# Optimization experiments

Hardware: AMD Instinct MI355X
Metric: run time of the kernel (lower is better)

## Reference

```python
import jax, jax.numpy as jnp
import numpy as np

# Module config (mirrors TritonMoEConfig)
N_EMBD = 768
EXPERT_SIZES = [(8, 512), (8, 1024)]  # (count, width) pairs
TOP_K = 8
NORM_TOPK_PROB = True

EXPERT_WIDTHS = []
for cnt, w in EXPERT_SIZES:
    EXPERT_WIDTHS += [w] * cnt
EXPERT_OFFSETS = np.concatenate([[0], np.cumsum(EXPERT_WIDTHS)]).astype(np.int64)
NUM_EXPERTS = len(EXPERT_WIDTHS)          # 16
TOTAL_WIDTH = int(EXPERT_OFFSETS[-1])     # 12288


def setup_inputs() -> dict:
    key = jax.random.key(0)
    k1, k2, k3, k4 = jax.random.split(key, 4)
    x = jax.random.normal(k1, (1, 2048, N_EMBD), dtype=jnp.float32)
    # trunc_normal(std=0.02) approximated by clipped normal
    router_w = jax.random.normal(k2, (NUM_EXPERTS, N_EMBD), dtype=jnp.float32) * 0.02
    w1 = jnp.clip(jax.random.normal(k3, (N_EMBD, TOTAL_WIDTH), dtype=jnp.float32) * 0.02, -0.06, 0.06)
    w2 = jnp.clip(jax.random.normal(k4, (TOTAL_WIDTH, N_EMBD), dtype=jnp.float32) * 0.02, -0.06, 0.06)
    return {"x": x, "router_w": router_w, "w1": w1, "w2": w2}


def reference(x, router_w, w1, w2):
    B, S, D = x.shape
    xt = x.reshape(-1, D)                              # [T, D]
    T = xt.shape[0]
    # 1. Route tokens: softmax over experts, top-k selection
    logits = jnp.einsum('td,ed->te', xt, router_w)     # [T, E]
    probs = jax.nn.softmax(logits, axis=-1)
    topk_w, topk_idx = jax.lax.top_k(probs, TOP_K)     # [T, K]
    if NORM_TOPK_PROB:
        topk_w = topk_w / jnp.sum(topk_w, axis=-1, keepdims=True)
    # Per-token combine weight for every expert (0 if not selected): [T, E]
    comb = jnp.zeros((T, NUM_EXPERTS), dtype=xt.dtype)
    comb = comb.at[jnp.arange(T)[:, None], topk_idx].add(topk_w)
    # 2-6. Grouped GEMM up (with activation) + down, combine with routing weights.
    # Experts have distinct widths, so loop over the fixed expert list.
    out = jnp.zeros_like(xt)
    for e in range(NUM_EXPERTS):
        off = int(EXPERT_OFFSETS[e])
        wd = EXPERT_WIDTHS[e]
        h = jax.nn.gelu(xt @ w1[:, off:off + wd])      # [T, wd]
        out = out + comb[:, e:e + 1] * (h @ w2[off:off + wd, :])
    return out.reshape(B, S, D)
```

## Files before the change

kernel.cpp:

```cpp
#include <hip/hip_runtime.h>
#include <hip/hip_bf16.h>


#define T_TOK 2048
#define D_EMB 768
#define W_TOT 12288
#define N_EXP 16

typedef __attribute__((ext_vector_type(4))) float f32x4;
typedef __attribute__((ext_vector_type(8))) short bf16x8;

typedef __attribute__((address_space(1))) const unsigned int as1c_u32;
typedef __attribute__((address_space(3))) unsigned int as3_u32;

__device__ __forceinline__ void gload16(const void* g, void* l) {
  __builtin_amdgcn_global_load_lds((as1c_u32*)g, (as3_u32*)l, 16, 0, 0);
}

__device__ __forceinline__ unsigned short f2bf(float f) {
  __hip_bfloat16 h = __float2bfloat16(f);
  return *reinterpret_cast<unsigned short*>(&h);
}

__device__ __forceinline__ float gelu_f(float x) {
  float x3 = x * x * x;
  float a = 0.7978845608028654f * __builtin_fmaf(0.044715f, x3, x);
  a = fminf(fmaxf(a, -20.f), 20.f);
  float e = __expf(-2.0f * a);
  float t = (1.0f - e) / (1.0f + e);
  return 0.5f * x * (1.0f + t);
}

__global__ __launch_bounds__(256) void transpose_cvt_kernel(
    const float* __restrict__ in, unsigned short* __restrict__ out, int R, int C) {
  __shared__ float tile[32][33];
  int c0 = blockIdx.x * 32;
  int r0 = blockIdx.y * 32;
  int i = threadIdx.x;
  {
    int r = i >> 3, c4 = (i & 7) * 4;
    float4 v = *(const float4*)(in + (size_t)(r0 + r) * C + c0 + c4);
    tile[r][c4 + 0] = v.x; tile[r][c4 + 1] = v.y;
    tile[r][c4 + 2] = v.z; tile[r][c4 + 3] = v.w;
  }
  __syncthreads();
  {
    int c = i >> 3, r4 = (i & 7) * 4;
    ushort4 o;
    o.x = f2bf(tile[r4 + 0][c]);
    o.y = f2bf(tile[r4 + 1][c]);
    o.z = f2bf(tile[r4 + 2][c]);
    o.w = f2bf(tile[r4 + 3][c]);
    *(ushort4*)(out + (size_t)(c0 + c) * R + r0 + r4) = o;
  }
}


__global__ __launch_bounds__(256) void router_kernel(
    const float* __restrict__ x, const float* __restrict__ rw,
    float* __restrict__ comb, unsigned short* __restrict__ xbout) {
  int tid = threadIdx.x, lane = tid & 63, w = tid >> 6;
  int t = blockIdx.x * 4 + w;
  const float* xr = x + (size_t)t * D_EMB;
  float xv[12];
#pragma unroll
  for (int i = 0; i < 12; ++i) xv[i] = xr[lane + 64 * i];
#pragma unroll
  for (int i = 0; i < 12; ++i)
    xbout[(size_t)t * D_EMB + lane + 64 * i] = f2bf(xv[i]);
  float lg[16];
#pragma unroll
  for (int e = 0; e < 16; ++e) {
    const float* we = rw + (size_t)e * D_EMB;
    float p = 0.f;
#pragma unroll
    for (int i = 0; i < 12; ++i) p = __builtin_fmaf(xv[i], we[lane + 64 * i], p);
#pragma unroll
    for (int off = 32; off >= 1; off >>= 1) p += __shfl_xor(p, off, 64);
    lg[e] = p;
  }
  float mx = lg[0];
#pragma unroll
  for (int e = 1; e < 16; ++e) mx = fmaxf(mx, lg[e]);
  float ex[16];
#pragma unroll
  for (int e = 0; e < 16; ++e) ex[e] = __expf(lg[e] - mx);
  float selsum = 0.f, myval = 0.f;
#pragma unroll
  for (int e = 0; e < 16; ++e) {
    int rank = 0;
#pragma unroll
    for (int e2 = 0; e2 < 16; ++e2)
      rank += (ex[e2] > ex[e]) || (ex[e2] == ex[e] && e2 < e);
    bool sel = rank < 8;
    float v = sel ? ex[e] : 0.f;
    selsum += v;
    if (e == lane) myval = v;
  }
  if (lane < 16) comb[(size_t)t * N_EXP + lane] = myval / selsum;
}


#define TILE(TT)                                                               \
  {                                                                            \
    asm volatile("s_waitcnt vmcnt(4)" ::: "memory");                           \
    __builtin_amdgcn_s_barrier();                                              \
    __builtin_amdgcn_sched_barrier(0);                                         \
    _Pragma("unroll")                                                          \
    for (int m = 0; m < 8; ++m)                                                \
      a[m] = *(const bf16x8*)(smem + (TT) * 16384 + abase + m * 1024);         \
    _Pragma("unroll")                                                          \
    for (int n = 0; n < 4; ++n)                                                \
      b[n] = *(const bf16x8*)(smem + 49152 + (TT) * 16384 + bbase + n * 1024); \
    gload16(pA0, smem + (((TT) + 2) % 3) * 16384 + wid * 1024);                \
    gload16(pA1, smem + (((TT) + 2) % 3) * 16384 + 8192 + wid * 1024);         \
    gload16(pB0, smem + 49152 + (((TT) + 2) % 3) * 16384 + wid * 1024);        \
    gload16(pB1, smem + 49152 + (((TT) + 2) % 3) * 16384 + 8192 + wid * 1024); \
    pA0 += 64; pA1 += 64; pB0 += 64; pB1 += 64;                                \
    __builtin_amdgcn_sched_barrier(0);                                         \
    __builtin_amdgcn_s_setprio(1);                                             \
    _Pragma("unroll")                                                          \
    for (int m = 0; m < 8; ++m)                                                \
      _Pragma("unroll")                                                        \
      for (int n = 0; n < 4; ++n)                                              \
        acc[m][n] = __builtin_amdgcn_mfma_f32_16x16x32_bf16(                   \
            a[m], b[n], acc[m][n], 0, 0, 0);                                   \
    __builtin_amdgcn_s_setprio(0);                                             \
  }

template <int EPI, int MAP>
__global__ __launch_bounds__(512, 2) void gemm_kernel(
    const unsigned short* __restrict__ Ag, const unsigned short* __restrict__ Bg,
    int lda, int ldb, int ntiles, int kchunk,
    const float* __restrict__ comb, unsigned short* __restrict__ hout,
    float* __restrict__ pout) {
  __shared__ __align__(16) char smem[98304];

  const int tid = threadIdx.x;
  const int lane = tid & 63;
  const int wid = tid >> 6;
  const int wr = wid >> 2;
  const int wc = wid & 3;

  int mt, nt, zt;
  {
    int bid = blockIdx.x;
    if (MAP == 0) {
      int xcd = bid & 7, r = bid >> 3;
      nt = xcd * 6 + (r >> 3); mt = r & 7; zt = 0;
    } else {
      zt = bid & 7; int r = bid >> 3;
      nt = r % 3; mt = r / 3;
    }
  }
  const int rm0 = mt * 256;
  const int cn0 = nt * 256;
  const int kbeg = zt * kchunk;

  const int srow = tid >> 2;
  const int scol = ((tid & 3) ^ (srow & 3)) << 4;
  const char* pA0 = (const char*)Ag + ((size_t)(rm0 + srow) * lda + kbeg) * 2 + scol;
  const char* pA1 = (const char*)Ag + ((size_t)(rm0 + 128 + srow) * lda + kbeg) * 2 + scol;
  const char* pB0 = (const char*)Bg + ((size_t)(cn0 + srow) * ldb + kbeg) * 2 + scol;
  const char* pB1 = (const char*)Bg + ((size_t)(cn0 + 128 + srow) * ldb + kbeg) * 2 + scol;

  const int colsw = ((lane >> 4) ^ (lane & 3)) << 4;
  const int abase = (wr * 128 + (lane & 15)) * 64 + colsw;
  const int bbase = (wc * 64 + (lane & 15)) * 64 + colsw;

  f32x4 acc[8][4];
#pragma unroll
  for (int m = 0; m < 8; ++m)
#pragma unroll
    for (int n = 0; n < 4; ++n) acc[m][n] = (f32x4){0.f, 0.f, 0.f, 0.f};

  gload16(pA0, smem + wid * 1024);
  gload16(pA1, smem + 8192 + wid * 1024);
  gload16(pB0, smem + 49152 + wid * 1024);
  gload16(pB1, smem + 49152 + 8192 + wid * 1024);
  gload16(pA0 + 64, smem + 16384 + wid * 1024);
  gload16(pA1 + 64, smem + 16384 + 8192 + wid * 1024);
  gload16(pB0 + 64, smem + 49152 + 16384 + wid * 1024);
  gload16(pB1 + 64, smem + 49152 + 16384 + 8192 + wid * 1024);
  pA0 += 128; pA1 += 128; pB0 += 128; pB1 += 128;
  __builtin_amdgcn_sched_barrier(0);

  bf16x8 a[8], b[4];
  const int nit = ntiles / 3;
  for (int i = 0; i < nit; ++i) {
    TILE(0)
    TILE(1)
    TILE(2)
  }

  asm volatile("s_waitcnt vmcnt(0)" ::: "memory");
  __syncthreads();

  const int r0 = (lane >> 4) * 4;
  const int cl = lane & 15;
  if constexpr (EPI == 1) {
    float* Cwf = (float*)smem;
    {
      int row = tid >> 1, c8 = (tid & 1) * 8;
      const float* s = comb + (size_t)(rm0 + row) * N_EXP + c8;
      *(float4*)&Cwf[row * 16 + c8] = *(const float4*)s;
      *(float4*)&Cwf[row * 16 + c8 + 4] = *(const float4*)(s + 4);
    }
    __syncthreads();
#pragma unroll
    for (int n = 0; n < 4; ++n) {
      int colg = cn0 + wc * 64 + n * 16 + cl;
      int e = (colg < 4096) ? (colg >> 9) : (8 + ((colg - 4096) >> 10));
#pragma unroll
      for (int m = 0; m < 8; ++m) {
        int rl = wr * 128 + m * 16 + r0;
#pragma unroll
        for (int r = 0; r < 4; ++r) {
          float v = gelu_f(acc[m][n][r]) * Cwf[(rl + r) * 16 + e];
          hout[(size_t)(rm0 + rl + r) * W_TOT + colg] = f2bf(v);
        }
      }
    }
  } else {
    float* pz = pout + (size_t)zt * T_TOK * D_EMB;
#pragma unroll
    for (int n = 0; n < 4; ++n) {
      int colg = cn0 + wc * 64 + n * 16 + cl;
#pragma unroll
      for (int m = 0; m < 8; ++m) {
        int rl = wr * 128 + m * 16 + r0;
#pragma unroll
        for (int r = 0; r < 4; ++r)
          pz[(size_t)(rm0 + rl + r) * D_EMB + colg] = acc[m][n][r];
      }
    }
  }
}

__global__ __launch_bounds__(256) void reduce_kernel(
    const float* __restrict__ partial, float* __restrict__ out, int splits) {
  int i = (blockIdx.x * 256 + threadIdx.x) * 4;
  if (i >= T_TOK * D_EMB) return;
  float4 s = *(const float4*)(partial + i);
  for (int sp = 1; sp < splits; ++sp) {
    float4 v = *(const float4*)(partial + (size_t)sp * T_TOK * D_EMB + i);
    s.x += v.x; s.y += v.y; s.z += v.z; s.w += v.w;
  }
  *(float4*)(out + i) = s;
}


extern "C" void kernel_launch(void* const* d_in, const int* in_sizes, int n_in,
                              void* d_out, int out_size, void* d_ws, size_t ws_size,
                              hipStream_t stream) {
  const float* x = (const float*)d_in[0];
  const float* router_w = (const float*)d_in[1];
  const float* w1 = (const float*)d_in[2];
  const float* w2 = (const float*)d_in[3];
  float* out = (float*)d_out;

  char* ws = (char*)d_ws;
  size_t off = 0;
  auto alloc = [&](size_t bytes) {
    char* p = ws + off;
    off += (bytes + 255) & ~(size_t)255;
    return p;
  };
  unsigned short* xb  = (unsigned short*)alloc((size_t)T_TOK * D_EMB * 2);
  unsigned short* w1t = (unsigned short*)alloc((size_t)W_TOT * D_EMB * 2);
  unsigned short* w2t = (unsigned short*)alloc((size_t)D_EMB * W_TOT * 2);
  unsigned short* h   = (unsigned short*)alloc((size_t)T_TOK * W_TOT * 2);
  float* comb         = (float*)alloc((size_t)T_TOK * N_EXP * 4);

  const int splits = 8;
  float* partial = (float*)alloc((size_t)splits * T_TOK * D_EMB * 4);
  int kchunk = W_TOT / splits;

  transpose_cvt_kernel<<<dim3(W_TOT / 32, D_EMB / 32), 256, 0, stream>>>(w1, w1t, D_EMB, W_TOT);
  transpose_cvt_kernel<<<dim3(D_EMB / 32, W_TOT / 32), 256, 0, stream>>>(w2, w2t, W_TOT, D_EMB);
  router_kernel<<<T_TOK / 4, 256, 0, stream>>>(x, router_w, comb, xb);

  gemm_kernel<1, 0><<<384, 512, 0, stream>>>(
      xb, w1t, D_EMB, D_EMB, D_EMB / 32, D_EMB, comb, h, nullptr);

  gemm_kernel<0, 1><<<192, 512, 0, stream>>>(
      h, w2t, W_TOT, W_TOT, kchunk / 32, kchunk, nullptr, nullptr, partial);

  reduce_kernel<<<(T_TOK * D_EMB) / 1024, 256, 0, stream>>>(partial, out, splits);
}
```

Before: 156.6 us.

## Restructure GEMM main loop into 64-wide K tiles with four-phase interleaved loads

The GEMM inner loop moves from a triple-buffered 32-wide K tile to a double-buffered 64-wide K tile (128 KB LDS). Each K tile is split into four MFMA quadrant phases, with global-to-LDS loads and LDS reads interleaved between barriers, in the style of the HipKittens 8-wave ping-pong schedule. Launch bounds drop to one block per CU to fit the larger LDS. The aim is to hide load latency behind MFMA work and halve the barrier count per K. In exchange there are more fine-grained barriers and lower occupancy, and the buffer reuse ordering is delicate.

```diff
diff --git a/kernel.cpp b/kernel.cpp
--- a/kernel.cpp
+++ b/kernel.cpp
@@ -101,40 +101,87 @@
 }
 
 
-#define TILE(TT)                                                               \
-  {                                                                            \
-    asm volatile("s_waitcnt vmcnt(4)" ::: "memory");                           \
-    __builtin_amdgcn_s_barrier();                                              \
-    __builtin_amdgcn_sched_barrier(0);                                         \
-    _Pragma("unroll")                                                          \
-    for (int m = 0; m < 8; ++m)                                                \
-      a[m] = *(const bf16x8*)(smem + (TT) * 16384 + abase + m * 1024);         \
-    _Pragma("unroll")                                                          \
-    for (int n = 0; n < 4; ++n)                                                \
-      b[n] = *(const bf16x8*)(smem + 49152 + (TT) * 16384 + bbase + n * 1024); \
-    gload16(pA0, smem + (((TT) + 2) % 3) * 16384 + wid * 1024);                \
-    gload16(pA1, smem + (((TT) + 2) % 3) * 16384 + 8192 + wid * 1024);         \
-    gload16(pB0, smem + 49152 + (((TT) + 2) % 3) * 16384 + wid * 1024);        \
-    gload16(pB1, smem + 49152 + (((TT) + 2) % 3) * 16384 + 8192 + wid * 1024); \
-    pA0 += 64; pA1 += 64; pB0 += 64; pB1 += 64;                                \
-    __builtin_amdgcn_sched_barrier(0);                                         \
-    __builtin_amdgcn_s_setprio(1);                                             \
-    _Pragma("unroll")                                                          \
-    for (int m = 0; m < 8; ++m)                                                \
-      _Pragma("unroll")                                                        \
-      for (int n = 0; n < 4; ++n)                                              \
-        acc[m][n] = __builtin_amdgcn_mfma_f32_16x16x32_bf16(                   \
-            a[m], b[n], acc[m][n], 0, 0, 0);                                   \
-    __builtin_amdgcn_s_setprio(0);                                             \
+#define MFMA8(AM, NN, A0, A1, B0, B1)                                           \
+  _Pragma("unroll") for (int m = 0; m < 4; ++m)                                 \
+    _Pragma("unroll") for (int n = 0; n < 2; ++n) {                             \
+      acc[(AM) + m][(NN) + n] = __builtin_amdgcn_mfma_f32_16x16x32_bf16(        \
+          A0[m], B0[n], acc[(AM) + m][(NN) + n], 0, 0, 0);                      \
+      acc[(AM) + m][(NN) + n] = __builtin_amdgcn_mfma_f32_16x16x32_bf16(        \
+          A1[m], B1[n], acc[(AM) + m][(NN) + n], 0, 0, 0);                      \
+    }
+
+#define KTILE(P)                                                                \
+  {                \
+    _Pragma("unroll") for (int m = 0; m < 4; ++m) {                             \
+      aC0[m] = *(const bf16x8*)(smem + (P)*32768 + ab0 + m * 2048);             \
+      aC1[m] = *(const bf16x8*)(smem + (P)*32768 + ab1 + m * 2048);             \
+    }                                                                           \
+    _Pragma("unroll") for (int n = 0; n < 2; ++n) {                             \
+      bL0[n] = *(const bf16x8*)(smem + 65536 + (P)*32768 + bb0 + n * 2048);     \
+      bL1[n] = *(const bf16x8*)(smem + 65536 + (P)*32768 + bb1 + n * 2048);     \
+    }                                                                           \
+    gload16(pA00 + (P)*128, smem + ((P)^1)*32768 + wid * 1024);                 \
+    gload16(pA01 + (P)*128, smem + ((P)^1)*32768 + 8192 + wid * 1024);          \
+    asm volatile("s_waitcnt lgkmcnt(8)" ::: "memory");                          \
+    __builtin_amdgcn_s_barrier();                                               \
+    asm volatile("s_waitcnt lgkmcnt(0)" ::: "memory");                          \
+    __builtin_amdgcn_sched_barrier(0);                                          \
+    __builtin_amdgcn_s_setprio(1);                                              \
+    MFMA8(0, 0, aC0, aC1, bL0, bL1)                                             \
+    __builtin_amdgcn_s_setprio(0);                                              \
+    __builtin_amdgcn_s_barrier();                                               \
+    __builtin_amdgcn_sched_barrier(0);                                          \
+                            \
+    _Pragma("unroll") for (int n = 0; n < 2; ++n) {                             \
+      bH0[n] = *(const bf16x8*)(smem + 65536 + (P)*32768 + bb0 + (2+n)*2048);   \
+      bH1[n] = *(const bf16x8*)(smem + 65536 + (P)*32768 + bb1 + (2+n)*2048);   \
+    }                                                                           \
+    gload16(pA10 + (P)*128, smem + ((P)^1)*32768 + 16384 + wid * 1024);         \
+    gload16(pA11 + (P)*128, smem + ((P)^1)*32768 + 24576 + wid * 1024);         \
+    __builtin_amdgcn_s_barrier();                                               \
+    asm volatile("s_waitcnt lgkmcnt(0)" ::: "memory");                          \
+    __builtin_amdgcn_sched_barrier(0);                                          \
+    __builtin_amdgcn_s_setprio(1);                                              \
+    MFMA8(0, 2, aC0, aC1, bH0, bH1)                                             \
+    __builtin_amdgcn_s_setprio(0);                                              \
+    __builtin_amdgcn_s_barrier();                                               \
+    __builtin_amdgcn_sched_barrier(0);                                          \
+      \
+                                                 \
+    _Pragma("unroll") for (int m = 0; m < 4; ++m) {                             \
+      aC0[m] = *(const bf16x8*)(smem + (P)*32768 + ab0 + 8192 + m * 2048);      \
+      aC1[m] = *(const bf16x8*)(smem + (P)*32768 + ab1 + 8192 + m * 2048);      \
+    }                                                                           \
+    gload16(pB00 + (P)*128, smem + 65536 + (P)*32768 + wid * 1024);             \
+    gload16(pB01 + (P)*128, smem + 65536 + (P)*32768 + 8192 + wid * 1024);      \
+    __builtin_amdgcn_s_barrier();                                               \
+    asm volatile("s_waitcnt lgkmcnt(0)" ::: "memory");                          \
+    __builtin_amdgcn_sched_barrier(0);                                          \
+    __builtin_amdgcn_s_setprio(1);                                              \
+    MFMA8(4, 2, aC0, aC1, bH0, bH1)                                             \
+    __builtin_amdgcn_s_setprio(0);                                              \
+    __builtin_amdgcn_s_barrier();                                               \
+    __builtin_amdgcn_sched_barrier(0);                                          \
+                 \
+    gload16(pB10 + (P)*128, smem + 65536 + (P)*32768 + 16384 + wid * 1024);     \
+    gload16(pB11 + (P)*128, smem + 65536 + (P)*32768 + 24576 + wid * 1024);     \
+    asm volatile("s_waitcnt vmcnt(4)" ::: "memory");                            \
+    __builtin_amdgcn_s_barrier();                                               \
+    __builtin_amdgcn_sched_barrier(0);                                          \
+    __builtin_amdgcn_s_setprio(1);                                              \
+    MFMA8(4, 0, aC0, aC1, bL0, bL1)                                             \
+    __builtin_amdgcn_s_setprio(0);                                              \
+    __builtin_amdgcn_s_barrier();                                               \
+    __builtin_amdgcn_sched_barrier(0);                                          \
   }
 
 template <int EPI, int MAP>
-__global__ __launch_bounds__(512, 2) void gemm_kernel(
+__global__ __launch_bounds__(512, 1) void gemm_kernel(
     const unsigned short* __restrict__ Ag, const unsigned short* __restrict__ Bg,
-    int lda, int ldb, int ntiles, int kchunk,
+    int lda, int ldb, int niter, int kchunk,
     const float* __restrict__ comb, unsigned short* __restrict__ hout,
     float* __restrict__ pout) {
-  __shared__ __align__(16) char smem[98304];
+  __shared__ __align__(16) char smem[131072];
 
   const int tid = threadIdx.x;
   const int lane = tid & 63;
@@ -157,16 +204,27 @@
   const int cn0 = nt * 256;
   const int kbeg = zt * kchunk;
 
-  const int srow = tid >> 2;
-  const int scol = ((tid & 3) ^ (srow & 3)) << 4;
-  const char* pA0 = (const char*)Ag + ((size_t)(rm0 + srow) * lda + kbeg) * 2 + scol;
-  const char* pA1 = (const char*)Ag + ((size_t)(rm0 + 128 + srow) * lda + kbeg) * 2 + scol;
-  const char* pB0 = (const char*)Bg + ((size_t)(cn0 + srow) * ldb + kbeg) * 2 + scol;
-  const char* pB1 = (const char*)Bg + ((size_t)(cn0 + 128 + srow) * ldb + kbeg) * 2 + scol;
-
-  const int colsw = ((lane >> 4) ^ (lane & 3)) << 4;
-  const int abase = (wr * 128 + (lane & 15)) * 64 + colsw;
-  const int bbase = (wc * 64 + (lane & 15)) * 64 + colsw;
+  auto gsrc = [&](const unsigned short* base, int ld, int row0, int h, int g) {
+    int row = row0 + h * 128 + g * 64 + (tid >> 3);
+    int scol = (((tid & 7) ^ ((tid >> 3) & 7)) << 4);
+    return (const char*)base + ((size_t)row * ld + kbeg) * 2 + scol;
+  };
+  const char* pA00 = gsrc(Ag, lda, rm0, 0, 0);
+  const char* pA01 = gsrc(Ag, lda, rm0, 0, 1);
+  const char* pA10 = gsrc(Ag, lda, rm0, 1, 0);
+  const char* pA11 = gsrc(Ag, lda, rm0, 1, 1);
+  const char* pB00 = gsrc(Bg, ldb, cn0, 0, 0);
+  const char* pB01 = gsrc(Bg, ldb, cn0, 0, 1);
+  const char* pB10 = gsrc(Bg, ldb, cn0, 1, 0);
+  const char* pB11 = gsrc(Bg, ldb, cn0, 1, 1);
+
+  const int lswz = (lane & 7) << 4;
+  const int colk0 = (((lane >> 4) & 3) * 16) ^ lswz;
+  const int colk1 = (64 + ((lane >> 4) & 3) * 16) ^ lswz;
+  const int ab0 = wr * 16384 + (lane & 15) * 128 + colk0;
+  const int ab1 = wr * 16384 + (lane & 15) * 128 + colk1;
+  const int bb0 = (wc >> 1) * 16384 + ((wc & 1) * 64 + (lane & 15)) * 128 + colk0;
+  const int bb1 = (wc >> 1) * 16384 + ((wc & 1) * 64 + (lane & 15)) * 128 + colk1;
 
   f32x4 acc[8][4];
 #pragma unroll
@@ -174,23 +232,30 @@
 #pragma unroll
     for (int n = 0; n < 4; ++n) acc[m][n] = (f32x4){0.f, 0.f, 0.f, 0.f};
 
-  gload16(pA0, smem + wid * 1024);
-  gload16(pA1, smem + 8192 + wid * 1024);
-  gload16(pB0, smem + 49152 + wid * 1024);
-  gload16(pB1, smem + 49152 + 8192 + wid * 1024);
-  gload16(pA0 + 64, smem + 16384 + wid * 1024);
-  gload16(pA1 + 64, smem + 16384 + 8192 + wid * 1024);
-  gload16(pB0 + 64, smem + 49152 + 16384 + wid * 1024);
-  gload16(pB1 + 64, smem + 49152 + 16384 + 8192 + wid * 1024);
-  pA0 += 128; pA1 += 128; pB0 += 128; pB1 += 128;
+  gload16(pA00, smem + wid * 1024);
+  gload16(pA01, smem + 8192 + wid * 1024);
+  gload16(pA10, smem + 16384 + wid * 1024);
+  gload16(pA11, smem + 24576 + wid * 1024);
+  gload16(pB00, smem + 65536 + wid * 1024);
+  gload16(pB01, smem + 65536 + 8192 + wid * 1024);
+  gload16(pB10, smem + 65536 + 16384 + wid * 1024);
+  gload16(pB11, smem + 65536 + 24576 + wid * 1024);
+  gload16(pB00 + 128, smem + 65536 + 32768 + wid * 1024);
+  gload16(pB01 + 128, smem + 65536 + 32768 + 8192 + wid * 1024);
+  gload16(pB10 + 128, smem + 65536 + 32768 + 16384 + wid * 1024);
+  gload16(pB11 + 128, smem + 65536 + 32768 + 24576 + wid * 1024);
+  pA00 += 128; pA01 += 128; pA10 += 128; pA11 += 128;
+  pB00 += 256; pB01 += 256; pB10 += 256; pB11 += 256;
+  asm volatile("s_waitcnt vmcnt(4)" ::: "memory");
+  __builtin_amdgcn_s_barrier();
   __builtin_amdgcn_sched_barrier(0);
 
-  bf16x8 a[8], b[4];
-  const int nit = ntiles / 3;
-  for (int i = 0; i < nit; ++i) {
-    TILE(0)
-    TILE(1)
-    TILE(2)
+  bf16x8 aC0[4], aC1[4], bL0[2], bL1[2], bH0[2], bH1[2];
+  for (int i = 0; i < niter; ++i) {
+    KTILE(0)
+    KTILE(1)
+    pA00 += 256; pA01 += 256; pA10 += 256; pA11 += 256;
+    pB00 += 256; pB01 += 256; pB10 += 256; pB11 += 256;
   }
 
   asm volatile("s_waitcnt vmcnt(0)" ::: "memory");
@@ -281,10 +346,10 @@
   router_kernel<<<T_TOK / 4, 256, 0, stream>>>(x, router_w, comb, xb);
 
   gemm_kernel<1, 0><<<384, 512, 0, stream>>>(
-      xb, w1t, D_EMB, D_EMB, D_EMB / 32, D_EMB, comb, h, nullptr);
+      xb, w1t, D_EMB, D_EMB, (D_EMB / 64) / 2, D_EMB, comb, h, nullptr);
 
   gemm_kernel<0, 1><<<192, 512, 0, stream>>>(
-      h, w2t, W_TOT, W_TOT, kchunk / 32, kchunk, nullptr, nullptr, partial);
+      h, w2t, W_TOT, W_TOT, (kchunk / 64) / 2, kchunk, nullptr, nullptr, partial);
 
   reduce_kernel<<<(T_TOK * D_EMB) / 1024, 256, 0, stream>>>(partial, out, splits);
 }
```

New measurement: 179.3 us. 1.14x slower.
